# Kernel tuning notes

Measured on AMD Instinct MI355X. Metric: run time of the kernel, lower is better.

The kernel has to match this reference:

```python
import jax, jax.numpy as jnp
import numpy as np

OUT = 7          # output_size
SR = 2           # sampling_ratio
IMG = 512.0      # image size (512, 512)
CANON_SCALE = 224.0
CANON_LVL = 4.0
LVL_MIN, LVL_MAX = 2, 6  # strides 4..64


def roi_align_level(feat, rois, scale):
    """torchvision roi_align (aligned=False) for all rois on one level.
    feat: [B,C,H,W], rois: [B,N,4] in image coords. Returns [B,N,C,7,7]."""
    B, C, H, W = feat.shape
    N = rois.shape[1]
    x1 = rois[..., 0] * scale
    y1 = rois[..., 1] * scale
    x2 = rois[..., 2] * scale
    y2 = rois[..., 3] * scale
    roi_w = jnp.maximum(x2 - x1, 1.0)
    roi_h = jnp.maximum(y2 - y1, 1.0)
    bin_w = roi_w / OUT
    bin_h = roi_h / OUT
    # 14 sample coordinates per axis: 7 bins x 2 samples, offset (i+0.5)/2 within bin
    grid = (jnp.arange(OUT, dtype=feat.dtype)[:, None]
            + (jnp.arange(SR, dtype=feat.dtype)[None, :] + 0.5) / SR).reshape(-1)  # [14]
    py = y1[..., None] + grid * bin_h[..., None]   # [B,N,14]
    px = x1[..., None] + grid * bin_w[..., None]   # [B,N,14]
    yy = py[..., :, None]                          # [B,N,14,1]
    xx = px[..., None, :]                          # [B,N,1,14]
    valid = (yy >= -1.0) & (yy <= H) & (xx >= -1.0) & (xx <= W)  # [B,N,14,14]
    y = jnp.clip(yy, 0.0, H - 1)
    x = jnp.clip(xx, 0.0, W - 1)
    y0f = jnp.floor(y)
    x0f = jnp.floor(x)
    ly = y - y0f   # [B,N,14,1]
    lx = x - x0f   # [B,N,1,14]
    y0 = y0f.astype(jnp.int32)
    x0 = x0f.astype(jnp.int32)
    y1i = jnp.minimum(y0 + 1, H - 1)
    x1i = jnp.minimum(x0 + 1, W - 1)

    flat = feat.reshape(B, C, H * W)

    def gather(yi, xi):
        idx = (yi * W + xi).reshape(B, -1)                     # [B, N*14*14]
        g = jax.vmap(lambda f, i: f[:, i])(flat, idx)          # [B, C, N*14*14]
        return g.reshape(B, C, N, SR * OUT, SR * OUT)

    w00 = ((1 - ly) * (1 - lx))[:, None]  # [B,1,N,14,14]
    w01 = ((1 - ly) * lx)[:, None]
    w10 = (ly * (1 - lx))[:, None]
    w11 = (ly * lx)[:, None]
    val = (gather(y0, x0) * w00 + gather(y0, x1i) * w01
           + gather(y1i, x0) * w10 + gather(y1i, x1i) * w11)
    val = val * valid[:, None].astype(feat.dtype)
    # average the SRxSR samples within each bin
    out = val.reshape(B, C, N, OUT, SR, OUT, SR).mean(axis=(4, 6))  # [B,C,N,7,7]
    return out.transpose(0, 2, 1, 3, 4)  # [B,N,C,7,7]


def setup_inputs() -> dict:
    key = jax.random.key(0)
    ks = jax.random.split(key, 6)
    B, C, N = 4, 256, 256
    feats = {}
    for lvl, hw in enumerate([128, 64, 32, 16, 8]):
        feats[f"feat{lvl}"] = jax.random.normal(ks[lvl], (B, C, hw, hw), dtype=jnp.float32)
    # random boxes inside the 512x512 image with x2>x1, y2>y1
    xy = jax.random.uniform(ks[5], (B, N, 2, 2), minval=0.0, maxval=IMG)
    lo = xy.min(axis=2)
    hi = xy.max(axis=2)
    rois = jnp.concatenate([lo, hi], axis=-1)  # [B,N,4] = (x1,y1,x2,y2)
    feats["rois"] = rois
    return feats


def reference(feat0, feat1, feat2, feat3, feat4, rois):
    B, N = rois.shape[0], rois.shape[1]
    feats = [feat0, feat1, feat2, feat3, feat4]
    scales = [0.25, 0.125, 0.0625, 0.03125, 0.015625]  # inferred from 128..8 vs 512
    # FPN level assignment (torchvision LevelMapper)
    area = (rois[..., 2] - rois[..., 0]) * (rois[..., 3] - rois[..., 1])
    lvl = jnp.floor(CANON_LVL + jnp.log2(jnp.sqrt(area) / CANON_SCALE + 1e-6))
    lvl = (jnp.clip(lvl, LVL_MIN, LVL_MAX) - LVL_MIN).astype(jnp.int32)  # [B,N] in 0..4
    # pool every roi on every level, then select its assigned level
    stacked = jnp.stack([roi_align_level(f, rois, s) for f, s in zip(feats, scales)],
                        axis=2)  # [B,N,5,C,7,7]
    sel = jnp.take_along_axis(stacked,
                              lvl[:, :, None, None, None, None].astype(jnp.int32),
                              axis=2)[:, :, 0]  # [B,N,C,7,7]
    B_, N_, C, _, _ = sel.shape
    return sel.reshape(B_ * N_, C, OUT, OUT)
```

## Files before the change

### kernel.cpp

```cpp
#include <hip/hip_runtime.h>

#define OUT 7
#define NB 4
#define NC 256
#define NN 256
#define EPR (NC * OUT * OUT)

typedef float nfloat4 __attribute__((ext_vector_type(4)));
typedef unsigned short nushort4 __attribute__((ext_vector_type(4)));
typedef unsigned short nushort2 __attribute__((ext_vector_type(2)));

__device__ inline unsigned short f2bf(float f) {
    unsigned u = __builtin_bit_cast(unsigned, f);
    u += 0x7FFFu + ((u >> 16) & 1u);
    return (unsigned short)(u >> 16);
}

__device__ inline float bf2f(unsigned short s) {
    return __builtin_bit_cast(float, (unsigned)s << 16);
}

__global__ __launch_bounds__(256) void transpose_all(
    const float* __restrict__ f0, const float* __restrict__ f1,
    const float* __restrict__ f2, const float* __restrict__ f3,
    const float* __restrict__ f4, unsigned short* __restrict__ T)
{
    __shared__ float tile[32][33];
    const int bx = blockIdx.x;

    const float* in; unsigned short* outp; int P, t, shp;
    if (bx < 4096)      { in = f0; outp = T;            P = 16384; t = bx;        shp = 9; }
    else if (bx < 5120) { in = f1; outp = T + 16777216; P = 4096;  t = bx - 4096; shp = 7; }
    else if (bx < 5376) { in = f2; outp = T + 20971520; P = 1024;  t = bx - 5120; shp = 5; }
    else if (bx < 5440) { in = f3; outp = T + 22020096; P = 256;   t = bx - 5376; shp = 3; }
    else                { in = f4; outp = T + 22282240; P = 64;    t = bx - 5440; shp = 1; }

    const int pt   = t & ((1 << shp) - 1);
    const int rest = t >> shp;
    const int cm   = rest & 1;
    const int b    = rest >> 1;
    const int p0   = pt << 5;
    const int tx   = threadIdx.x & 7;
    const int ty   = threadIdx.x >> 3;

    #pragma unroll
    for (int ct = 0; ct < 4; ++ct) {
        const int c0 = (cm << 7) + (ct << 5);
        const float* src = in + ((size_t)((b << 8) + c0 + ty)) * P + p0 + (tx << 2);
        nfloat4 v = __builtin_nontemporal_load((const nfloat4*)src);
        tile[ty][tx * 4 + 0] = v.x;
        tile[ty][tx * 4 + 1] = v.y;
        tile[ty][tx * 4 + 2] = v.z;
        tile[ty][tx * 4 + 3] = v.w;
        __syncthreads();

        nushort4 w;
        w.x = f2bf(tile[4 * tx + 0][ty]);
        w.y = f2bf(tile[4 * tx + 1][ty]);
        w.z = f2bf(tile[4 * tx + 2][ty]);
        w.w = f2bf(tile[4 * tx + 3][ty]);
        unsigned short* dst = outp + ((size_t)b * P + p0 + ty) * NC + c0 + (tx << 2);
        *(nushort4*)dst = w;
        __syncthreads();
    }
}

__global__ __launch_bounds__(256, 5) void msroi_fast(
    const unsigned short* __restrict__ T, const float* __restrict__ rois,
    float* __restrict__ out)
{
    const int j     = ((blockIdx.x & 7) << 8) + (blockIdx.x >> 3);
    const int roi   = j >> 1;
    const int chunk = j & 1;
    const int tid   = threadIdx.x;

    __shared__ float s_wy[2][14];
    __shared__ float s_wx[2][14];
    __shared__ int   s_yr[2][14];
    __shared__ int   s_xc[2][14];
    __shared__ int   s_lvl;
    __shared__ __align__(16) float s_out[128 * 49];

    if (tid < 28) {
        const float rx1 = rois[roi * 4 + 0];
        const float ry1 = rois[roi * 4 + 1];
        const float rx2 = rois[roi * 4 + 2];
        const float ry2 = rois[roi * 4 + 3];

        float area = (rx2 - rx1) * (ry2 - ry1);
        float lf = floorf(4.0f + log2f(sqrtf(area) / 224.0f + 1e-6f));
        lf = fminf(fmaxf(lf, 2.0f), 6.0f);
        int lvl = (int)lf - 2;
        if (tid == 0) s_lvl = lvl;

        float scale = 1.0f / (float)(4 << lvl);
        int   W     = 128 >> lvl;

        float x1 = rx1 * scale, y1 = ry1 * scale;
        float x2 = rx2 * scale, y2 = ry2 * scale;
        float rw = fmaxf(x2 - x1, 1.0f);
        float rh = fmaxf(y2 - y1, 1.0f);
        float bw = rw / (float)OUT;
        float bh = rh / (float)OUT;

        bool isx = (tid >= 14);
        int  g   = isx ? tid - 14 : tid;
        float gv = ((float)g + 0.5f) * 0.5f;
        float p  = isx ? (x1 + gv * bw) : (y1 + gv * bh);

        float v = (p >= -1.0f && p <= (float)W) ? 1.0f : 0.0f;
        float pc  = fminf(fmaxf(p, 0.0f), (float)(W - 1));
        float p0f = floorf(pc);
        int   p0  = (int)p0f;
        int   p1  = min(p0 + 1, W - 1);
        float l   = pc - p0f;

        if (isx) {
            s_xc[0][g] = p0; s_xc[1][g] = p1;
            s_wx[0][g] = v * (1.0f - l); s_wx[1][g] = v * l;
        } else {
            s_yr[0][g] = p0 * W; s_yr[1][g] = p1 * W;
            s_wy[0][g] = v * (1.0f - l); s_wy[1][g] = v * l;
        }
    }
    __syncthreads();

    const int lvl = s_lvl;
    const int W   = 128 >> lvl;
    const int POS = W * W;
    const int off_tab[5] = {0, 16777216, 20971520, 22020096, 22282240};
    const int b    = roi >> 8;
    const int q    = tid >> 6;
    const int cl   = (tid & 63) << 1;
    const unsigned short* base =
        T + (size_t)off_tab[lvl] + (size_t)b * POS * NC + (chunk << 7) + cl;

    auto make_off = [&](int p, int* off) {
        const int oy = p / 7;
        const int ox = p - oy * 7;
        const int R[4] = { s_yr[0][2 * oy],     s_yr[1][2 * oy],
                           s_yr[0][2 * oy + 1], s_yr[1][2 * oy + 1] };
        const int C[4] = { s_xc[0][2 * ox],     s_xc[1][2 * ox],
                           s_xc[0][2 * ox + 1], s_xc[1][2 * ox + 1] };
        #pragma unroll
        for (int a = 0; a < 4; ++a)
            #pragma unroll
            for (int c2 = 0; c2 < 4; ++c2)
                off[a * 4 + c2] = R[a] + C[c2];
    };

    int p_cur = min(q * 13, 48);
    int offA[16];
    nushort2 L[16], M[16];
    make_off(p_cur, offA);
    #pragma unroll
    for (int k = 0; k < 16; ++k)
        L[k] = *(const nushort2*)&base[(size_t)offA[k] << 8];

    #pragma unroll
    for (int i = 0; i < 13; ++i) {
        const int p_nxt = min(q * 13 + i + 1, 48);
        if (i < 12) {
            int offB[16];
            make_off(p_nxt, offB);
            #pragma unroll
            for (int k = 0; k < 16; ++k)
                M[k] = *(const nushort2*)&base[(size_t)offB[k] << 8];
        }

        const int oy = p_cur / 7;
        const int ox = p_cur - oy * 7;
        const float WY[4] = { s_wy[0][2 * oy],     s_wy[1][2 * oy],
                              s_wy[0][2 * oy + 1], s_wy[1][2 * oy + 1] };
        const float WX[4] = { s_wx[0][2 * ox],     s_wx[1][2 * ox],
                              s_wx[0][2 * ox + 1], s_wx[1][2 * ox + 1] };

        float a0 = 0.0f, a1 = 0.0f;
        #pragma unroll
        for (int k = 0; k < 16; ++k) {
            const float w = WY[k >> 2] * WX[k & 3];
            a0 += w * bf2f(L[k].x);
            a1 += w * bf2f(L[k].y);
        }

        s_out[(cl + 0) * 49 + p_cur] = a0 * 0.25f;
        s_out[(cl + 1) * 49 + p_cur] = a1 * 0.25f;

        #pragma unroll
        for (int k = 0; k < 16; ++k) L[k] = M[k];
        p_cur = p_nxt;
    }
    __syncthreads();

    float* ob = out + (size_t)roi * EPR + (chunk << 7) * 49;
    #pragma unroll
    for (int k = 0; k < 6; ++k) {
        const int f = (tid + (k << 8)) << 2;
        nfloat4 v = *(const nfloat4*)&s_out[f];
        __builtin_nontemporal_store(v, (nfloat4*)&ob[f]);
    }
    if (tid < 32) {
        const int f = (tid + 1536) << 2;
        nfloat4 v = *(const nfloat4*)&s_out[f];
        __builtin_nontemporal_store(v, (nfloat4*)&ob[f]);
    }
}

__global__ __launch_bounds__(256) void msroi_kernel(
    const float* __restrict__ f0, const float* __restrict__ f1,
    const float* __restrict__ f2, const float* __restrict__ f3,
    const float* __restrict__ f4, const float* __restrict__ rois,
    float* __restrict__ out)
{
    const int roi = blockIdx.y;
    const int tid = threadIdx.x;

    __shared__ float s_wyt[14], s_wyb[14];
    __shared__ float s_wxl[14], s_wxr[14];
    __shared__ int   s_oy0[14], s_oy1[14];
    __shared__ int   s_x0[14],  s_x1[14];
    __shared__ int   s_lvl;

    if (tid < 28) {
        const float rx1 = rois[roi * 4 + 0];
        const float ry1 = rois[roi * 4 + 1];
        const float rx2 = rois[roi * 4 + 2];
        const float ry2 = rois[roi * 4 + 3];

        float area = (rx2 - rx1) * (ry2 - ry1);
        float lf = floorf(4.0f + log2f(sqrtf(area) / 224.0f + 1e-6f));
        lf = fminf(fmaxf(lf, 2.0f), 6.0f);
        int lvl = (int)lf - 2;
        if (tid == 0) s_lvl = lvl;

        float scale = 1.0f / (float)(4 << lvl);
        int   HW    = 128 >> lvl;

        float x1 = rx1 * scale, y1 = ry1 * scale;
        float x2 = rx2 * scale, y2 = ry2 * scale;
        float rw = fmaxf(x2 - x1, 1.0f);
        float rh = fmaxf(y2 - y1, 1.0f);
        float bw = rw / (float)OUT;
        float bh = rh / (float)OUT;

        bool isx = (tid >= 14);
        int  g   = isx ? tid - 14 : tid;
        float gv = ((float)g + 0.5f) * 0.5f;
        float p  = isx ? (x1 + gv * bw) : (y1 + gv * bh);

        float v = (p >= -1.0f && p <= (float)HW) ? 1.0f : 0.0f;
        float pc  = fminf(fmaxf(p, 0.0f), (float)(HW - 1));
        float p0f = floorf(pc);
        int   p0  = (int)p0f;
        int   p1  = min(p0 + 1, HW - 1);
        float l   = pc - p0f;

        if (isx) {
            s_x0[g] = p0; s_x1[g] = p1;
            s_wxl[g] = v * (1.0f - l); s_wxr[g] = v * l;
        } else {
            s_oy0[g] = p0 * HW; s_oy1[g] = p1 * HW;
            s_wyt[g] = v * (1.0f - l); s_wyb[g] = v * l;
        }
    }
    __syncthreads();

    const int lvl = s_lvl;
    const int HW  = 128 >> lvl;
    const int HW2 = HW * HW;
    const float* f = (lvl == 0) ? f0 : (lvl == 1) ? f1 : (lvl == 2) ? f2
                     : (lvl == 3) ? f3 : f4;
    const int b = roi >> 8;

    const int e0 = blockIdx.x * 512 + tid;

    float acc[2];
    #pragma unroll
    for (int k = 0; k < 2; ++k) {
        const int e  = e0 + k * 256;
        const int ec = (e < EPR) ? e : 0;
        const int c  = ec / 49;
        const int s  = ec - 49 * c;
        const int oy = s / 7;
        const int ox = s - 7 * oy;

        const float* fp = f + (size_t)(b * NC + c) * (size_t)HW2;

        float a = 0.0f;
        #pragma unroll
        for (int iy = 0; iy < 2; ++iy) {
            const int gy = oy * 2 + iy;
            const float wt = s_wyt[gy], wb = s_wyb[gy];
            const int   o0 = s_oy0[gy], o1 = s_oy1[gy];
            #pragma unroll
            for (int ix = 0; ix < 2; ++ix) {
                const int gx = ox * 2 + ix;
                const float wl = s_wxl[gx], wr = s_wxr[gx];
                const int   x0 = s_x0[gx],  x1i = s_x1[gx];
                const float v00 = fp[o0 + x0];
                const float v01 = fp[o0 + x1i];
                const float v10 = fp[o1 + x0];
                const float v11 = fp[o1 + x1i];
                a += (wt * wl) * v00 + (wt * wr) * v01
                   + (wb * wl) * v10 + (wb * wr) * v11;
            }
        }
        acc[k] = a * 0.25f;
    }

    #pragma unroll
    for (int k = 0; k < 2; ++k) {
        const int e = e0 + k * 256;
        if (e < EPR)
            __builtin_nontemporal_store(acc[k], &out[(size_t)roi * EPR + e]);
    }
}

extern "C" void kernel_launch(void* const* d_in, const int* in_sizes, int n_in,
                              void* d_out, int out_size, void* d_ws, size_t ws_size,
                              hipStream_t stream) {
    const float* f0   = (const float*)d_in[0];
    const float* f1   = (const float*)d_in[1];
    const float* f2   = (const float*)d_in[2];
    const float* f3   = (const float*)d_in[3];
    const float* f4   = (const float*)d_in[4];
    const float* rois = (const float*)d_in[5];
    float* out = (float*)d_out;

    const size_t need = 22347776ull * 2ull;
    if (ws_size >= need) {
        unsigned short* T = (unsigned short*)d_ws;
        transpose_all<<<dim3(5456), dim3(256), 0, stream>>>(f0, f1, f2, f3, f4, T);
        msroi_fast<<<dim3(NB * NN * 2), dim3(256), 0, stream>>>(T, rois, out);
    } else {
        dim3 grid((EPR + 511) / 512, NB * NN);
        dim3 block(256);
        msroi_kernel<<<grid, block, 0, stream>>>(f0, f1, f2, f3, f4, rois, out);
    }
}
```

Measured before the change: 163.3 us.

## Skip transposing level-0 features and sample them directly from NCHW input

The largest feature level is no longer transposed to a channels-last bf16 buffer. ROIs assigned to level 0 now gather directly from the original fp32 NCHW tensor, one channel per thread pair, while the other levels keep the transposed path. This removes most of the transpose pre-pass traffic, since level 0 holds about three quarters of the feature data. In exchange, level-0 gathers become scattered per-channel loads rather than coalesced channel-contiguous loads. Only a fraction of ROIs land on level 0.

```diff
diff --git a/kernel.cpp b/kernel.cpp
--- a/kernel.cpp
+++ b/kernel.cpp
@@ -20,20 +20,19 @@
     return __builtin_bit_cast(float, (unsigned)s << 16);
 }
 
-__global__ __launch_bounds__(256) void transpose_all(
-    const float* __restrict__ f0, const float* __restrict__ f1,
-    const float* __restrict__ f2, const float* __restrict__ f3,
-    const float* __restrict__ f4, unsigned short* __restrict__ T)
+__global__ __launch_bounds__(256) void transpose_rest(
+    const float* __restrict__ f1, const float* __restrict__ f2,
+    const float* __restrict__ f3, const float* __restrict__ f4,
+    unsigned short* __restrict__ T)
 {
     __shared__ float tile[32][33];
     const int bx = blockIdx.x;
 
     const float* in; unsigned short* outp; int P, t, shp;
-    if (bx < 4096)      { in = f0; outp = T;            P = 16384; t = bx;        shp = 9; }
-    else if (bx < 5120) { in = f1; outp = T + 16777216; P = 4096;  t = bx - 4096; shp = 7; }
-    else if (bx < 5376) { in = f2; outp = T + 20971520; P = 1024;  t = bx - 5120; shp = 5; }
-    else if (bx < 5440) { in = f3; outp = T + 22020096; P = 256;   t = bx - 5376; shp = 3; }
-    else                { in = f4; outp = T + 22282240; P = 64;    t = bx - 5440; shp = 1; }
+    if (bx < 1024)      { in = f1; outp = T;           P = 4096; t = bx;        shp = 7; }
+    else if (bx < 1280) { in = f2; outp = T + 4194304; P = 1024; t = bx - 1024; shp = 5; }
+    else if (bx < 1344) { in = f3; outp = T + 5242880; P = 256;  t = bx - 1280; shp = 3; }
+    else                { in = f4; outp = T + 5505024; P = 64;   t = bx - 1344; shp = 1; }
 
     const int pt   = t & ((1 << shp) - 1);
     const int rest = t >> shp;
@@ -66,8 +65,8 @@
 }
 
 __global__ __launch_bounds__(256, 5) void msroi_fast(
-    const unsigned short* __restrict__ T, const float* __restrict__ rois,
-    float* __restrict__ out)
+    const unsigned short* __restrict__ T, const float* __restrict__ f0,
+    const float* __restrict__ rois, float* __restrict__ out)
 {
     const int j     = ((blockIdx.x & 7) << 8) + (blockIdx.x >> 3);
     const int roi   = j >> 1;
@@ -126,69 +125,96 @@
     __syncthreads();
 
     const int lvl = s_lvl;
-    const int W   = 128 >> lvl;
-    const int POS = W * W;
-    const int off_tab[5] = {0, 16777216, 20971520, 22020096, 22282240};
-    const int b    = roi >> 8;
-    const int q    = tid >> 6;
-    const int cl   = (tid & 63) << 1;
-    const unsigned short* base =
-        T + (size_t)off_tab[lvl] + (size_t)b * POS * NC + (chunk << 7) + cl;
-
-    auto make_off = [&](int p, int* off) {
-        const int oy = p / 7;
-        const int ox = p - oy * 7;
-        const int R[4] = { s_yr[0][2 * oy],     s_yr[1][2 * oy],
-                           s_yr[0][2 * oy + 1], s_yr[1][2 * oy + 1] };
-        const int C[4] = { s_xc[0][2 * ox],     s_xc[1][2 * ox],
-                           s_xc[0][2 * ox + 1], s_xc[1][2 * ox + 1] };
+    const int b   = roi >> 8;
+
+    if (lvl == 0) {
+        const int cloc = tid >> 1;
+        const int half = tid & 1;
+        const float* fpp =
+            f0 + (size_t)((b << 8) + (chunk << 7) + cloc) * 16384;
+        const int pbeg = half ? 25 : 0;
+        const int pend = half ? 49 : 25;
+        for (int p = pbeg; p < pend; ++p) {
+            const int oy = p / 7;
+            const int ox = p - oy * 7;
+            float acc = 0.0f;
+            #pragma unroll
+            for (int a = 0; a < 4; ++a) {
+                const int   yr = s_yr[a & 1][2 * oy + (a >> 1)];
+                const float wy = s_wy[a & 1][2 * oy + (a >> 1)];
+                #pragma unroll
+                for (int c2 = 0; c2 < 4; ++c2) {
+                    const int   xc = s_xc[c2 & 1][2 * ox + (c2 >> 1)];
+                    const float wx = s_wx[c2 & 1][2 * ox + (c2 >> 1)];
+                    acc += (wy * wx) * fpp[yr + xc];
+                }
+            }
+            s_out[cloc * 49 + p] = acc * 0.25f;
+        }
+    } else {
+        const int W   = 128 >> lvl;
+        const int POS = W * W;
+        const int off_tab[5] = {0, 0, 4194304, 5242880, 5505024};
+        const int q    = tid >> 6;
+        const int cl   = (tid & 63) << 1;
+        const unsigned short* base =
+            T + (size_t)off_tab[lvl] + (size_t)b * POS * NC + (chunk << 7) + cl;
+
+        auto make_off = [&](int p, int* off) {
+            const int oy = p / 7;
+            const int ox = p - oy * 7;
+            const int R[4] = { s_yr[0][2 * oy],     s_yr[1][2 * oy],
+                               s_yr[0][2 * oy + 1], s_yr[1][2 * oy + 1] };
+            const int C[4] = { s_xc[0][2 * ox],     s_xc[1][2 * ox],
+                               s_xc[0][2 * ox + 1], s_xc[1][2 * ox + 1] };
+            #pragma unroll
+            for (int a = 0; a < 4; ++a)
+                #pragma unroll
+                for (int c2 = 0; c2 < 4; ++c2)
+                    off[a * 4 + c2] = R[a] + C[c2];
+        };
+
+        int p_cur = min(q * 13, 48);
+        int offA[16];
+        nushort2 L[16], M[16];
+        make_off(p_cur, offA);
         #pragma unroll
-        for (int a = 0; a < 4; ++a)
-            #pragma unroll
-            for (int c2 = 0; c2 < 4; ++c2)
-                off[a * 4 + c2] = R[a] + C[c2];
-    };
-
-    int p_cur = min(q * 13, 48);
-    int offA[16];
-    nushort2 L[16], M[16];
-    make_off(p_cur, offA);
-    #pragma unroll
-    for (int k = 0; k < 16; ++k)
-        L[k] = *(const nushort2*)&base[(size_t)offA[k] << 8];
-
-    #pragma unroll
-    for (int i = 0; i < 13; ++i) {
-        const int p_nxt = min(q * 13 + i + 1, 48);
-        if (i < 12) {
-            int offB[16];
-            make_off(p_nxt, offB);
-            #pragma unroll
-            for (int k = 0; k < 16; ++k)
-                M[k] = *(const nushort2*)&base[(size_t)offB[k] << 8];
-        }
-
-        const int oy = p_cur / 7;
-        const int ox = p_cur - oy * 7;
-        const float WY[4] = { s_wy[0][2 * oy],     s_wy[1][2 * oy],
-                              s_wy[0][2 * oy + 1], s_wy[1][2 * oy + 1] };
-        const float WX[4] = { s_wx[0][2 * ox],     s_wx[1][2 * ox],
-                              s_wx[0][2 * ox + 1], s_wx[1][2 * ox + 1] };
-
-        float a0 = 0.0f, a1 = 0.0f;
+        for (int k = 0; k < 16; ++k)
+            L[k] = *(const nushort2*)&base[(size_t)offA[k] << 8];
+
         #pragma unroll
-        for (int k = 0; k < 16; ++k) {
-            const float w = WY[k >> 2] * WX[k & 3];
-            a0 += w * bf2f(L[k].x);
-            a1 += w * bf2f(L[k].y);
-        }
-
-        s_out[(cl + 0) * 49 + p_cur] = a0 * 0.25f;
-        s_out[(cl + 1) * 49 + p_cur] = a1 * 0.25f;
-
-        #pragma unroll
-        for (int k = 0; k < 16; ++k) L[k] = M[k];
-        p_cur = p_nxt;
+        for (int i = 0; i < 13; ++i) {
+            const int p_nxt = min(q * 13 + i + 1, 48);
+            if (i < 12) {
+                int offB[16];
+                make_off(p_nxt, offB);
+                #pragma unroll
+                for (int k = 0; k < 16; ++k)
+                    M[k] = *(const nushort2*)&base[(size_t)offB[k] << 8];
+            }
+
+            const int oy = p_cur / 7;
+            const int ox = p_cur - oy * 7;
+            const float WY[4] = { s_wy[0][2 * oy],     s_wy[1][2 * oy],
+                                  s_wy[0][2 * oy + 1], s_wy[1][2 * oy + 1] };
+            const float WX[4] = { s_wx[0][2 * ox],     s_wx[1][2 * ox],
+                                  s_wx[0][2 * ox + 1], s_wx[1][2 * ox + 1] };
+
+            float a0 = 0.0f, a1 = 0.0f;
+            #pragma unroll
+            for (int k = 0; k < 16; ++k) {
+                const float w = WY[k >> 2] * WX[k & 3];
+                a0 += w * bf2f(L[k].x);
+                a1 += w * bf2f(L[k].y);
+            }
+
+            s_out[(cl + 0) * 49 + p_cur] = a0 * 0.25f;
+            s_out[(cl + 1) * 49 + p_cur] = a1 * 0.25f;
+
+            #pragma unroll
+            for (int k = 0; k < 16; ++k) L[k] = M[k];
+            p_cur = p_nxt;
+        }
     }
     __syncthreads();
 
@@ -327,11 +353,11 @@
     const float* rois = (const float*)d_in[5];
     float* out = (float*)d_out;
 
-    const size_t need = 22347776ull * 2ull;
+    const size_t need = 5570560ull * 2ull;
     if (ws_size >= need) {
         unsigned short* T = (unsigned short*)d_ws;
-        transpose_all<<<dim3(5456), dim3(256), 0, stream>>>(f0, f1, f2, f3, f4, T);
-        msroi_fast<<<dim3(NB * NN * 2), dim3(256), 0, stream>>>(T, rois, out);
+        transpose_rest<<<dim3(1360), dim3(256), 0, stream>>>(f1, f2, f3, f4, T);
+        msroi_fast<<<dim3(NB * NN * 2), dim3(256), 0, stream>>>(T, f0, rois, out);
     } else {
         dim3 grid((EPR + 511) / 512, NB * NN);
         dim3 block(256);
```

After: 501.4 us. 207% more time.
